# Kernel tuning notes

Measured on AMD Instinct MI355X. Metric: run time of the kernel, lower is better.

Reference implementation:

```python
import jax, jax.numpy as jnp
import numpy as np

NQ = 8
NL = 3
DIM = 2 ** NQ


def _rx(psi, w, theta):
    # theta: scalar or [B]
    B = psi.shape[0]
    t = jnp.atleast_1d(theta).astype(jnp.float32)
    c = jnp.cos(t / 2)[:, None, None].astype(jnp.complex64)
    s = (-1j * jnp.sin(t / 2))[:, None, None].astype(jnp.complex64)
    p = psi.reshape(B, 2 ** w, 2, -1)
    s0, s1 = p[:, :, 0], p[:, :, 1]
    return jnp.stack([c * s0 + s * s1, s * s0 + c * s1], axis=2).reshape(B, DIM)


def _ry(psi, w, theta):
    B = psi.shape[0]
    t = jnp.atleast_1d(theta).astype(jnp.float32)
    c = jnp.cos(t / 2)[:, None, None].astype(jnp.complex64)
    s = jnp.sin(t / 2)[:, None, None].astype(jnp.complex64)
    p = psi.reshape(B, 2 ** w, 2, -1)
    s0, s1 = p[:, :, 0], p[:, :, 1]
    return jnp.stack([c * s0 - s * s1, s * s0 + c * s1], axis=2).reshape(B, DIM)


def _rz(psi, w, theta):
    B = psi.shape[0]
    t = jnp.atleast_1d(theta).astype(jnp.float32)
    e0 = jnp.exp(-0.5j * t.astype(jnp.complex64))[:, None, None]
    e1 = jnp.exp(0.5j * t.astype(jnp.complex64))[:, None, None]
    p = psi.reshape(B, 2 ** w, 2, -1)
    return jnp.stack([e0 * p[:, :, 0], e1 * p[:, :, 1]], axis=2).reshape(B, DIM)


def _cnot(psi, c, t):
    # control c, target t (wire 0 = most significant axis)
    B = psi.shape[0]
    a, b = (c, t) if c < t else (t, c)
    p = psi.reshape(B, 2 ** a, 2, 2 ** (b - a - 1), 2, -1)
    caxis = 2 if c < t else 4
    taxis = 4 if c < t else 2
    idx = [slice(None)] * 6
    idx[caxis] = 1
    sub = p[tuple(idx)]  # control=1 slab, caxis removed
    fl_axis = taxis - (1 if taxis > caxis else 0)
    p = p.at[tuple(idx)].set(jnp.flip(sub, axis=fl_axis))
    return p.reshape(B, DIM)


# PauliZ signs per wire: [NQ, 2^NQ]
_bits = (np.arange(DIM)[None, :] >> (NQ - 1 - np.arange(NQ)[:, None])) & 1
_Z_SIGNS = jnp.asarray((1 - 2 * _bits).astype(np.float32))


def _quantum_layer(enc, qrx, qry, qrz):
    # enc: [B, NQ] encoding angles; qrx/qry/qrz: [NL, NQ] scalar params
    B = enc.shape[0]
    psi = jnp.zeros((B, DIM), jnp.complex64).at[:, 0].set(1.0)
    for i in range(NQ):
        psi = _rx(psi, i, enc[:, i])
    for l in range(NL):
        for i in range(NQ):
            psi = _rx(psi, i, qrx[l, i])
            psi = _ry(psi, i, qry[l, i])
            psi = _rz(psi, i, qrz[l, i])
        for i in range(NQ - 1):
            psi = _cnot(psi, i, i + 1)
        psi = _cnot(psi, NQ - 1, 0)
    probs = psi.real ** 2 + psi.imag ** 2  # [B, 2^NQ]
    return probs @ _Z_SIGNS.T  # [B, NQ] <Z_i>


def _critic(x, w1, b1, w2, b2, qrx, qry, qrz, w3, b3, w4, b4):
    h = jax.nn.relu(x @ w1 + b1)
    enc = h @ w2 + b2
    ex = _quantum_layer(enc, qrx, qry, qrz)
    h2 = jax.nn.relu(ex @ w3 + b3)
    return h2 @ w4 + b4


def setup_inputs() -> dict:
    key = jax.random.key(0)
    ks = jax.random.split(key, 32)
    B, OBS, ACT, H = 65536, 96, 32, 256
    D = OBS + ACT

    def lin(k, fin, fout):
        return jax.random.normal(k, (fin, fout), jnp.float32) * (1.0 / np.sqrt(fin))

    inp = {
        'state': jax.random.normal(ks[0], (B, OBS), jnp.float32),
        'action': jax.random.normal(ks[1], (B, ACT), jnp.float32),
    }
    for ci, tag in enumerate(['a', 'b']):
        o = 2 + ci * 15
        inp['w1' + tag] = lin(ks[o + 0], D, H)
        inp['b1' + tag] = jnp.zeros((H,), jnp.float32)
        inp['w2' + tag] = lin(ks[o + 1], H, NQ)
        inp['b2' + tag] = jnp.zeros((NQ,), jnp.float32)
        inp['qrx' + tag] = jax.random.normal(ks[o + 2], (NL, NQ), jnp.float32)
        inp['qry' + tag] = jax.random.normal(ks[o + 3], (NL, NQ), jnp.float32)
        inp['qrz' + tag] = jax.random.normal(ks[o + 4], (NL, NQ), jnp.float32)
        inp['w3' + tag] = lin(ks[o + 5], NQ, H)
        inp['b3' + tag] = jnp.zeros((H,), jnp.float32)
        inp['w4' + tag] = lin(ks[o + 6], H, 1)
        inp['b4' + tag] = jnp.zeros((1,), jnp.float32)
    return inp


def reference(state, action,
              w1a, b1a, w2a, b2a, qrxa, qrya, qrza, w3a, b3a, w4a, b4a,
              w1b, b1b, w2b, b2b, qrxb, qryb, qrzb, w3b, b3b, w4b, b4b):
    x = jnp.concatenate([state, action], axis=1)
    q1 = _critic(x, w1a, b1a, w2a, b2a, qrxa, qrya, qrza, w3a, b3a, w4a, b4a)
    q2 = _critic(x, w1b, b1b, w2b, b2b, qrxb, qryb, qrzb, w3b, b3b, w4b, b4b)
    return (q1, q2)
```

## Files before the change

kernel.cpp:

```cpp
#include <hip/hip_runtime.h>
#include <math.h>


typedef __attribute__((ext_vector_type(8))) short bfrag_t;
typedef __attribute__((ext_vector_type(16))) float accv_t;

__device__ __forceinline__ unsigned short f2bf(float x) {
  unsigned u = __float_as_uint(x);
  u += 0x7FFFu + ((u >> 16) & 1u);
  return (unsigned short)(u >> 16);
}
__device__ __forceinline__ float bf2f(unsigned short h) {
  return __uint_as_float(((unsigned)h) << 16);
}
__device__ __forceinline__ unsigned pack2(float a, float b) {
  return (unsigned)f2bf(a) | ((unsigned)f2bf(b) << 16);
}

struct C2 { float r, i; };
__device__ __forceinline__ C2 cmul(C2 a, C2 b){ return C2{a.r*b.r - a.i*b.i, a.r*b.i + a.i*b.r}; }
__device__ __forceinline__ C2 cadd(C2 a, C2 b){ return C2{a.r+b.r, a.i+b.i}; }

#define APPLY2(A,Bx)                                                        \
  { float ar=re[A], ai=im[A], br=re[Bx], bi=im[Bx];                         \
    re[A]  = u00r*ar - u00i*ai + u01r*br - u01i*bi;                         \
    im[A]  = u00r*ai + u00i*ar + u01r*bi + u01i*br;                         \
    re[Bx] = u10r*ar - u10i*ai + u11r*br - u11i*bi;                         \
    im[Bx] = u10r*ai + u10i*ar + u11r*bi + u11i*br; }

__global__ __launch_bounds__(256)
void prep_weights(const float* __restrict__ qrxa, const float* __restrict__ qrya,
                  const float* __restrict__ qrza,
                  const float* __restrict__ qrxb, const float* __restrict__ qryb,
                  const float* __restrict__ qrzb,
                  const float* __restrict__ w1a, const float* __restrict__ w1b,
                  const float* __restrict__ w2a, const float* __restrict__ w2b,
                  const float* __restrict__ w3a, const float* __restrict__ w3b,
                  unsigned short* __restrict__ Bm, unsigned short* __restrict__ Gm,
                  unsigned short* __restrict__ w1p, unsigned short* __restrict__ w2p) {
  int blk = blockIdx.x;
  int tid = threadIdx.x;
  if (blk < 128) {
    __shared__ float sg[192];
    int c = blk >> 6;
    if (tid < 24) {
      const float* qx = c ? qrxb : qrxa;
      const float* qy = c ? qryb : qrya;
      const float* qz = c ? qrzb : qrza;
      int g = tid;
      float tx = 0.5f*qx[g], ty = 0.5f*qy[g], tz = 0.5f*qz[g];
      float cx = cosf(tx), sx = sinf(tx);
      float cy = cosf(ty), sy = sinf(ty);
      float cz = cosf(tz), sz = sinf(tz);
      C2 rx00{cx,0.f}, rx01{0.f,-sx}, rx10{0.f,-sx}, rx11{cx,0.f};
      C2 m00 = cadd(cmul(C2{cy,0.f},rx00), cmul(C2{-sy,0.f},rx10));
      C2 m01 = cadd(cmul(C2{cy,0.f},rx01), cmul(C2{-sy,0.f},rx11));
      C2 m10 = cadd(cmul(C2{sy,0.f},rx00), cmul(C2{cy,0.f},rx10));
      C2 m11 = cadd(cmul(C2{sy,0.f},rx01), cmul(C2{cy,0.f},rx11));
      C2 e0{cz,-sz}, e1{cz,sz};
      C2 u00 = cmul(e0,m00), u01 = cmul(e0,m01), u10 = cmul(e1,m10), u11 = cmul(e1,m11);
      float* o = sg + g*8;
      o[0]=u00.r; o[1]=u00.i; o[2]=u01.r; o[3]=u01.i;
      o[4]=u10.r; o[5]=u10.i; o[6]=u11.r; o[7]=u11.i;
    }
    __syncthreads();
    int lane = tid & 63;
    int wid = blk*4 + (tid >> 6);
    int bcol = wid & 255;
    int p = __popc(bcol) & 3;
    float phr = (p==0) ? 1.f : ((p==2) ? -1.f : 0.f);
    float phi = (p==1) ? -1.f : ((p==3) ? 1.f : 0.f);
    float re[4], im[4];
    #pragma unroll
    for (int j = 0; j < 4; ++j) {
      int idx = 4*lane + j;
      re[j] = (idx==bcol) ? phr : 0.f;
      im[j] = (idx==bcol) ? phi : 0.f;
    }
    #pragma unroll
    for (int l = 0; l < 3; ++l) {
      #pragma unroll
      for (int q = 0; q < 8; ++q) {
        const float* u = &sg[(size_t)(l*8 + q)*8];
        float u00r=u[0],u00i=u[1],u01r=u[2],u01i=u[3];
        float u10r=u[4],u10i=u[5],u11r=u[6],u11i=u[7];
        if (q < 6) {
          int m = 5-q, mask = 1<<m;
          bool s1 = ((lane >> m) & 1) != 0;
          float udr = s1?u11r:u00r, udi = s1?u11i:u00i;
          float uor = s1?u10r:u01r, uoi = s1?u10i:u01i;
          #pragma unroll
          for (int j = 0; j < 4; ++j) {
            float pr = __shfl_xor(re[j], mask);
            float pi = __shfl_xor(im[j], mask);
            float nr = udr*re[j] - udi*im[j] + uor*pr - uoi*pi;
            float ni = udr*im[j] + udi*re[j] + uor*pi + uoi*pr;
            re[j]=nr; im[j]=ni;
          }
        } else if (q == 6) { APPLY2(0,2); APPLY2(1,3); }
        else               { APPLY2(0,1); APPLY2(2,3); }
      }
      #pragma unroll
      for (int cq = 0; cq <= 4; ++cq) {
        int tmask = 1 << (4-cq);
        bool pred = ((lane >> (5-cq)) & 1) != 0;
        #pragma unroll
        for (int j = 0; j < 4; ++j) {
          float sr = __shfl_xor(re[j], tmask);
          float si = __shfl_xor(im[j], tmask);
          re[j] = pred ? sr : re[j];
          im[j] = pred ? si : im[j];
        }
      }
      { bool pred = (lane & 1) != 0;
        float t0, t1;
        t0 = pred?re[2]:re[0]; t1 = pred?re[0]:re[2]; re[0]=t0; re[2]=t1;
        t0 = pred?im[2]:im[0]; t1 = pred?im[0]:im[2]; im[0]=t0; im[2]=t1;
        t0 = pred?re[3]:re[1]; t1 = pred?re[1]:re[3]; re[1]=t0; re[3]=t1;
        t0 = pred?im[3]:im[1]; t1 = pred?im[1]:im[3]; im[1]=t0; im[3]=t1; }
      { float t;
        t=re[2]; re[2]=re[3]; re[3]=t;
        t=im[2]; im[2]=im[3]; im[3]=t; }
      { re[1]=__shfl_xor(re[1],32); im[1]=__shfl_xor(im[1],32);
        re[3]=__shfl_xor(re[3],32); im[3]=__shfl_xor(im[3],32); }
    }
    #pragma unroll
    for (int j = 0; j < 4; ++j) {
      int i = 4*lane + j;
      Bm[(size_t)(c*512 + i)*256 + bcol]       = f2bf(re[j]);
      Bm[(size_t)(c*512 + 256 + i)*256 + bcol] = f2bf(im[j]);
    }
  } else if (blk < 192) {
    int slot = (blk-128)*256 + tid;
    int n = slot & 255, h5 = (slot>>8)&1, ks = (slot>>9)&7, p = (slot>>12)&1, c = slot>>13;
    const float* w1c = c ? w1b : w1a;
    #pragma unroll
    for (int j = 0; j < 8; ++j) {
      float v = w1c[(size_t)(ks*16 + h5*8 + j)*256 + n];
      unsigned short hi = f2bf(v);
      w1p[(size_t)slot*8 + j] = p ? f2bf(v - bf2f(hi)) : hi;
    }
  } else if (blk < 200) {
    int slot = (blk-192)*256 + tid;
    int combo = slot >> 4, part = slot & 15;
    int h5 = combo&1, k16 = (combo>>1)&15, p = (combo>>5)&1, c = (combo>>6)&1;
    const float* w2c = c ? w2b : w2a;
    #pragma unroll
    for (int jj = 0; jj < 16; ++jj) {
      int idx = part*16 + jj;
      int il = idx >> 3, j = idx & 7;
      int n = k16*16 + h5*8 + j;
      float v = (il < 8) ? w2c[(size_t)n*8 + il] : 0.f;
      unsigned short hi = f2bf(v);
      w2p[(size_t)combo*256 + idx] = p ? f2bf(v - bf2f(hi)) : hi;
    }
  } else {
    int idx = (blk-200)*256 + tid;
    int c = idx >> 16, w = (idx >> 13) & 7, ks = (idx >> 9) & 15;
    int l = (idx >> 3) & 63, j = idx & 7;
    int n = 32*w + (l & 31);
    int i = ks*16 + (l >> 5)*8 + j;
    const float* w3 = c ? w3b : w3a;
    float s = 0.f;
    #pragma unroll
    for (int q = 0; q < 8; ++q) {
      float sg2 = ((i >> (7-q)) & 1) ? -1.f : 1.f;
      s += sg2 * w3[q*256 + n];
    }
    Gm[idx] = f2bf(s);
  }
}

__global__ __launch_bounds__(256, 2)
void enc_mfma(const float* __restrict__ state, const float* __restrict__ action,
              const unsigned short* __restrict__ w1p,
              const float* __restrict__ b1a, const float* __restrict__ b1b,
              const unsigned short* __restrict__ w2p,
              const float* __restrict__ b2a, const float* __restrict__ b2b,
              float* __restrict__ enc, int Bn) {
  __shared__ __align__(16) char Bx[2][16384];
  __shared__ __align__(16) float sb1[2][256];
  __shared__ float sb2[2][8];
  __shared__ __align__(16) float encw[4][2][32][8];
  int tid = threadIdx.x;
  int lane = tid & 63, w = tid >> 6, il = lane & 31, h5 = lane >> 5;
  int r0 = blockIdx.x * 64;

  sb1[0][tid] = b1a[tid];
  sb1[1][tid] = b1b[tid];
  if (tid < 8) { sb2[0][tid] = b2a[tid]; sb2[1][tid] = b2b[tid]; }

  {
    int m = tid >> 2, kq = tid & 3;
    const float4* st4 = (const float4*)state;
    const float4* ac4 = (const float4*)action;
    #pragma unroll
    for (int ks = 0; ks < 8; ++ks) {
      float4 v = (ks < 6) ? st4[(size_t)(r0+m)*24 + ks*4 + kq]
                          : ac4[(size_t)(r0+m)*8 + (ks-6)*4 + kq];
      unsigned short hx = f2bf(v.x), hy = f2bf(v.y), hz = f2bf(v.z), hw = f2bf(v.w);
      uint2 hh, ll;
      hh.x = (unsigned)hx | ((unsigned)hy << 16);
      hh.y = (unsigned)hz | ((unsigned)hw << 16);
      ll.x = (unsigned)f2bf(v.x - bf2f(hx)) | ((unsigned)f2bf(v.y - bf2f(hy)) << 16);
      ll.y = (unsigned)f2bf(v.z - bf2f(hz)) | ((unsigned)f2bf(v.w - bf2f(hw)) << 16);
      int off = ks*2048 + m*32 + kq*8;
      *(uint2*)(&Bx[0][off]) = hh;
      *(uint2*)(&Bx[1][off]) = ll;
    }
  }
  __syncthreads();

  for (int c = 0; c < 2; ++c) {
    accv_t A[2][2] = {{{},{}},{{},{}}};
    #pragma unroll
    for (int ks = 0; ks < 8; ++ks) {
      bfrag_t a0h, a0l, a1h, a1l;
      {
        size_t b0 = ((size_t)((c*2+0)*8 + ks)*2 + h5)*256;
        size_t b1 = ((size_t)((c*2+1)*8 + ks)*2 + h5)*256;
        int t0 = 2*w, t1 = 2*w+1;
        a0h = *(const bfrag_t*)(w1p + (b0 + t0*32 + il)*8);
        a0l = *(const bfrag_t*)(w1p + (b1 + t0*32 + il)*8);
        a1h = *(const bfrag_t*)(w1p + (b0 + t1*32 + il)*8);
        a1l = *(const bfrag_t*)(w1p + (b1 + t1*32 + il)*8);
      }
      bfrag_t b0h = *(const bfrag_t*)(&Bx[0][ks*2048 + il*32 + h5*16]);
      bfrag_t b0l = *(const bfrag_t*)(&Bx[1][ks*2048 + il*32 + h5*16]);
      bfrag_t b1h_ = *(const bfrag_t*)(&Bx[0][ks*2048 + (32+il)*32 + h5*16]);
      bfrag_t b1l_ = *(const bfrag_t*)(&Bx[1][ks*2048 + (32+il)*32 + h5*16]);
      A[0][0] = __builtin_amdgcn_mfma_f32_32x32x16_bf16(a0h, b0h, A[0][0], 0,0,0);
      A[0][0] = __builtin_amdgcn_mfma_f32_32x32x16_bf16(a0h, b0l, A[0][0], 0,0,0);
      A[0][0] = __builtin_amdgcn_mfma_f32_32x32x16_bf16(a0l, b0h, A[0][0], 0,0,0);
      A[0][1] = __builtin_amdgcn_mfma_f32_32x32x16_bf16(a0h, b1h_, A[0][1], 0,0,0);
      A[0][1] = __builtin_amdgcn_mfma_f32_32x32x16_bf16(a0h, b1l_, A[0][1], 0,0,0);
      A[0][1] = __builtin_amdgcn_mfma_f32_32x32x16_bf16(a0l, b1h_, A[0][1], 0,0,0);
      A[1][0] = __builtin_amdgcn_mfma_f32_32x32x16_bf16(a1h, b0h, A[1][0], 0,0,0);
      A[1][0] = __builtin_amdgcn_mfma_f32_32x32x16_bf16(a1h, b0l, A[1][0], 0,0,0);
      A[1][0] = __builtin_amdgcn_mfma_f32_32x32x16_bf16(a1l, b0h, A[1][0], 0,0,0);
      A[1][1] = __builtin_amdgcn_mfma_f32_32x32x16_bf16(a1h, b1h_, A[1][1], 0,0,0);
      A[1][1] = __builtin_amdgcn_mfma_f32_32x32x16_bf16(a1h, b1l_, A[1][1], 0,0,0);
      A[1][1] = __builtin_amdgcn_mfma_f32_32x32x16_bf16(a1l, b1h_, A[1][1], 0,0,0);
    }
    #pragma unroll
    for (int nt = 0; nt < 2; ++nt) {
      #pragma unroll
      for (int g = 0; g < 4; ++g) {
        float4 bb = *(const float4*)&sb1[c][(2*w+nt)*32 + 8*g + 4*h5];
        float bba[4] = {bb.x, bb.y, bb.z, bb.w};
        #pragma unroll
        for (int jj = 0; jj < 4; ++jj) {
          A[nt][0][4*g+jj] = fmaxf(A[nt][0][4*g+jj] + bba[jj], 0.f);
          A[nt][1][4*g+jj] = fmaxf(A[nt][1][4*g+jj] + bba[jj], 0.f);
        }
      }
    }
    accv_t Cm[2] = {{},{}};
    #pragma unroll
    for (int k2 = 0; k2 < 4; ++k2) {
      int k16 = 4*w + k2;
      bfrag_t g2h = *(const bfrag_t*)(w2p + ((size_t)((c*2+0)*16 + k16)*2 + h5)*256 + il*8);
      bfrag_t g2l = *(const bfrag_t*)(w2p + ((size_t)((c*2+1)*16 + k16)*2 + h5)*256 + il*8);
      #pragma unroll
      for (int mt = 0; mt < 2; ++mt) {
        unsigned ph[2][2], pl[2][2];
        #pragma unroll
        for (int gi = 0; gi < 2; ++gi) {
          int G = 2*k2 + gi, nt = G >> 2, g = G & 3;
          float f0 = A[nt][mt][4*g+0], f1 = A[nt][mt][4*g+1];
          float f2 = A[nt][mt][4*g+2], f3 = A[nt][mt][4*g+3];
          unsigned short h0 = f2bf(f0), h1 = f2bf(f1), h2 = f2bf(f2), h3 = f2bf(f3);
          ph[gi][0] = (unsigned)h0 | ((unsigned)h1 << 16);
          ph[gi][1] = (unsigned)h2 | ((unsigned)h3 << 16);
          pl[gi][0] = (unsigned)f2bf(f0 - bf2f(h0)) | ((unsigned)f2bf(f1 - bf2f(h1)) << 16);
          pl[gi][1] = (unsigned)f2bf(f2 - bf2f(h2)) | ((unsigned)f2bf(f3 - bf2f(h3)) << 16);
        }
        union { bfrag_t v; unsigned u[4]; } FH, FL;
        #pragma unroll
        for (int r = 0; r < 2; ++r) {
          unsigned own_h = h5 ? ph[1][r] : ph[0][r];
          unsigned alt_h = h5 ? ph[0][r] : ph[1][r];
          unsigned rec_h = __shfl_xor((int)alt_h, 32);
          FH.u[r]   = h5 ? rec_h : own_h;
          FH.u[2+r] = h5 ? own_h : rec_h;
          unsigned own_l = h5 ? pl[1][r] : pl[0][r];
          unsigned alt_l = h5 ? pl[0][r] : pl[1][r];
          unsigned rec_l = __shfl_xor((int)alt_l, 32);
          FL.u[r]   = h5 ? rec_l : own_l;
          FL.u[2+r] = h5 ? own_l : rec_l;
        }
        Cm[mt] = __builtin_amdgcn_mfma_f32_32x32x16_bf16(g2h, FH.v, Cm[mt], 0,0,0);
        Cm[mt] = __builtin_amdgcn_mfma_f32_32x32x16_bf16(g2h, FL.v, Cm[mt], 0,0,0);
        Cm[mt] = __builtin_amdgcn_mfma_f32_32x32x16_bf16(g2l, FH.v, Cm[mt], 0,0,0);
      }
    }
    *(float4*)&encw[w][0][il][4*h5] = make_float4(Cm[0][0], Cm[0][1], Cm[0][2], Cm[0][3]);
    *(float4*)&encw[w][1][il][4*h5] = make_float4(Cm[1][0], Cm[1][1], Cm[1][2], Cm[1][3]);
    __syncthreads();
    #pragma unroll
    for (int half = 0; half < 2; ++half) {
      int s = tid + half*256;
      int e = s & 7, mm = s >> 3;
      float v = sb2[c][e];
      #pragma unroll
      for (int ww = 0; ww < 4; ++ww) v += encw[ww][mm>>5][mm&31][e];
      enc[((size_t)c*Bn + r0 + mm)*8 + e] = v;
    }
    __syncthreads();
  }
}

__global__ __launch_bounds__(512, 2)
void qgemm(const float* __restrict__ enc,
           const unsigned short* __restrict__ Bm, const unsigned short* __restrict__ Gm,
           const float* __restrict__ b3a, const float* __restrict__ w4a, const float* __restrict__ b4a,
           const float* __restrict__ b3b, const float* __restrict__ w4b, const float* __restrict__ b4b,
           float* __restrict__ out, int Bn) {
  __shared__ __align__(16) char APq[32768];
  char* Alds = APq;
  char* Plds = APq + 16384;
  float* qtmp = (float*)APq;

  int tid = threadIdx.x;
  int lane = tid & 63;
  int w = tid >> 6;
  int il = lane & 31;
  int h5 = lane >> 5;

  int c = blockIdx.x >> 7;
  int rowblock = blockIdx.x & 127;
  int rowsPerBlock = Bn >> 7;
  int subtiles = rowsPerBlock >> 5;

  bfrag_t bf0[16], bf1[16];
  {
    const unsigned short* base = Bm + ((size_t)(c*512 + 32*w + il)*256 + h5*8);
    #pragma unroll
    for (int ks = 0; ks < 16; ++ks) {
      bf0[ks] = *(const bfrag_t*)(base + ks*16);
      bf1[ks] = *(const bfrag_t*)(base + 256*256 + ks*16);
    }
  }
  int n2 = 32*w + il;
  const float* b3c = c ? b3b : b3a;
  const float* w4c = c ? w4b : w4a;
  const float* b4c = c ? b4b : b4a;
  float b3v = b3c[n2];
  float w4v = w4c[n2];
  float b4v = b4c[0];
  const unsigned short* Gbase = Gm + ((size_t)(c*8 + w)*16)*512 + lane*8;
  int pwbase = (n2>>4)*1024 + ((n2>>3)&1)*512 + (n2&7)*2;
  int rowAdd = 4*h5;

  for (int st = 0; st < subtiles; ++st) {
    int r0 = rowblock*rowsPerBlock + st*32;
    __syncthreads();
    {
      int m = tid & 31, g2 = tid >> 5;
      const float* ep = enc + ((size_t)c*Bn + r0 + m)*8;
      float4 ea = *(const float4*)ep;
      float4 eb = *(const float4*)(ep + 4);
      float c0,s0,c1,s1,c2,s2,c3,s3,c4,s4,c5,s5,c6,s6,c7,s7;
      __sincosf(0.5f*ea.x, &s0, &c0);
      __sincosf(0.5f*ea.y, &s1, &c1);
      __sincosf(0.5f*ea.z, &s2, &c2);
      __sincosf(0.5f*ea.w, &s3, &c3);
      __sincosf(0.5f*eb.x, &s4, &c4);
      __sincosf(0.5f*eb.y, &s5, &c5);
      __sincosf(0.5f*eb.z, &s6, &c6);
      __sincosf(0.5f*eb.w, &s7, &c7);
      float v0 = (g2&8) ? s0 : c0;
      float v1 = (g2&4) ? s1 : c1;
      float v2 = (g2&2) ? s2 : c2;
      float v3 = (g2&1) ? s3 : c3;
      float top = v0*v1*v2*v3;
      float hA = top*c4, hB = top*s4;
      float p67[4];
      p67[0] = c6*c7; p67[1] = c6*s7; p67[2] = s6*c7; p67[3] = s6*s7;
      float low[8];
      #pragma unroll
      for (int j = 0; j < 8; ++j) low[j] = ((j&4) ? s5 : c5) * p67[j&3];
      union { bfrag_t v; unsigned u[4]; } pk;
      #pragma unroll
      for (int k = 0; k < 4; ++k) pk.u[k] = pack2(hA*low[2*k], hA*low[2*k+1]);
      *(bfrag_t*)(Alds + g2*1024 + m*16) = pk.v;
      #pragma unroll
      for (int k = 0; k < 4; ++k) pk.u[k] = pack2(hB*low[2*k], hB*low[2*k+1]);
      *(bfrag_t*)(Alds + g2*1024 + 512 + m*16) = pk.v;
    }
    __syncthreads();
    accv_t acc0 = {}, acc1 = {};
    #pragma unroll
    for (int ks = 0; ks < 16; ++ks) {
      bfrag_t af = *(const bfrag_t*)(Alds + ks*1024 + lane*16);
      acc0 = __builtin_amdgcn_mfma_f32_32x32x16_bf16(af, bf0[ks], acc0, 0, 0, 0);
      acc1 = __builtin_amdgcn_mfma_f32_32x32x16_bf16(af, bf1[ks], acc1, 0, 0, 0);
    }
    #pragma unroll
    for (int r = 0; r < 16; ++r) {
      float P = acc0[r]*acc0[r] + acc1[r]*acc1[r];
      int row = (r&3) + 8*(r>>2) + rowAdd;
      *(unsigned short*)(Plds + pwbase + row*16) = f2bf(P);
    }
    __syncthreads();
    accv_t acc2 = {};
    #pragma unroll 4
    for (int ks = 0; ks < 16; ++ks) {
      bfrag_t pf = *(const bfrag_t*)(Plds + ks*1024 + lane*16);
      bfrag_t gf = *(const bfrag_t*)(Gbase + ks*512);
      acc2 = __builtin_amdgcn_mfma_f32_32x32x16_bf16(pf, gf, acc2, 0, 0, 0);
    }
    float qp[16];
    #pragma unroll
    for (int r = 0; r < 16; ++r) qp[r] = fmaxf(acc2[r] + b3v, 0.f) * w4v;
    __syncthreads();
    #pragma unroll
    for (int r = 0; r < 16; ++r) {
      int row = (r&3) + 8*(r>>2) + rowAdd;
      qtmp[row*256 + n2] = qp[r];
    }
    __syncthreads();
    {
      int row = tid >> 4, seg = tid & 15;
      const float4* qp4 = (const float4*)(qtmp + row*256 + seg*16);
      float4 a0 = qp4[0], a1 = qp4[1], a2 = qp4[2], a3 = qp4[3];
      float s = (a0.x+a0.y+a0.z+a0.w) + (a1.x+a1.y+a1.z+a1.w)
              + (a2.x+a2.y+a2.z+a2.w) + (a3.x+a3.y+a3.z+a3.w);
      s += __shfl_xor(s, 1);
      s += __shfl_xor(s, 2);
      s += __shfl_xor(s, 4);
      s += __shfl_xor(s, 8);
      if (seg == 0) out[(size_t)c*Bn + r0 + row] = s + b4v;
    }
  }
}

extern "C" void kernel_launch(void* const* d_in, const int* in_sizes, int n_in,
                              void* d_out, int out_size, void* d_ws, size_t ws_size,
                              hipStream_t stream) {
  (void)n_in; (void)out_size; (void)ws_size;
  const float* state  = (const float*)d_in[0];
  const float* action = (const float*)d_in[1];
  const float* w1a=(const float*)d_in[2];  const float* b1a=(const float*)d_in[3];
  const float* w2a=(const float*)d_in[4];  const float* b2a=(const float*)d_in[5];
  const float* qrxa=(const float*)d_in[6]; const float* qrya=(const float*)d_in[7];
  const float* qrza=(const float*)d_in[8];
  const float* w3a=(const float*)d_in[9];  const float* b3a=(const float*)d_in[10];
  const float* w4a=(const float*)d_in[11]; const float* b4a=(const float*)d_in[12];
  const float* w1b=(const float*)d_in[13]; const float* b1b=(const float*)d_in[14];
  const float* w2b=(const float*)d_in[15]; const float* b2b=(const float*)d_in[16];
  const float* qrxb=(const float*)d_in[17];const float* qryb=(const float*)d_in[18];
  const float* qrzb=(const float*)d_in[19];
  const float* w3b=(const float*)d_in[20]; const float* b3b=(const float*)d_in[21];
  const float* w4b=(const float*)d_in[22]; const float* b4b=(const float*)d_in[23];

  int B = in_sizes[0] / 96;
  char* wsb = (char*)d_ws;
  unsigned short* Bmat = (unsigned short*)(wsb);
  unsigned short* Gmat = (unsigned short*)(wsb + 524288);
  unsigned short* w1p  = (unsigned short*)(wsb + 786432);
  unsigned short* w2p  = (unsigned short*)(wsb + 1048576);
  float* enc           = (float*)(wsb + 1114112);

  prep_weights<<<712, 256, 0, stream>>>(qrxa,qrya,qrza,qrxb,qryb,qrzb,
                                        w1a,w1b,w2a,w2b,w3a,w3b,
                                        Bmat,Gmat,w1p,w2p);
  enc_mfma<<<B/64, 256, 0, stream>>>(state,action,w1p,b1a,b1b,w2p,b2a,b2b,enc,B);
  qgemm<<<256, 512, 0, stream>>>(enc, Bmat, Gmat, b3a, w4a, b4a, b3b, w4b, b4b,
                                 (float*)d_out, B);
}
```

Measured before the change: 226.4 us.

## Double qgemm grid, pad LDS tiles, prefetch enc rows, de-conflict reduction reads

The qgemm launch grows from 256 to 512 blocks, so each block handles half as many rows and more of the GPU's compute units get work. LDS row strides go from 1024 to 1056 bytes to reduce bank conflicts on the A and P tiles. The enc loads for the next subtile are issued right after the barrier so their latency overlaps the MFMA work. The final row reduction now uses an interleaved float4 pattern to avoid LDS conflicts. In exchange, each block reloads the 32 B-fragments per register, doubling the total B-matrix traffic, and it needs slightly more LDS.

```diff
diff --git a/kernel.cpp b/kernel.cpp
--- a/kernel.cpp
+++ b/kernel.cpp
@@ -316,9 +316,9 @@
            const float* __restrict__ b3a, const float* __restrict__ w4a, const float* __restrict__ b4a,
            const float* __restrict__ b3b, const float* __restrict__ w4b, const float* __restrict__ b4b,
            float* __restrict__ out, int Bn) {
-  __shared__ __align__(16) char APq[32768];
+  __shared__ __align__(16) char APq[33792];
   char* Alds = APq;
-  char* Plds = APq + 16384;
+  char* Plds = APq + 16896;
   float* qtmp = (float*)APq;
 
   int tid = threadIdx.x;
@@ -327,9 +327,9 @@
   int il = lane & 31;
   int h5 = lane >> 5;
 
-  int c = blockIdx.x >> 7;
-  int rowblock = blockIdx.x & 127;
-  int rowsPerBlock = Bn >> 7;
+  int c = blockIdx.x >> 8;
+  int rowblock = blockIdx.x & 255;
+  int rowsPerBlock = Bn >> 8;
   int subtiles = rowsPerBlock >> 5;
 
   bfrag_t bf0[16], bf1[16];
@@ -349,17 +349,22 @@
   float w4v = w4c[n2];
   float b4v = b4c[0];
   const unsigned short* Gbase = Gm + ((size_t)(c*8 + w)*16)*512 + lane*8;
-  int pwbase = (n2>>4)*1024 + ((n2>>3)&1)*512 + (n2&7)*2;
+  int pwbase = (n2>>4)*1056 + ((n2>>3)&1)*512 + (n2&7)*2;
   int rowAdd = 4*h5;
+
+  int am = tid & 31, ag2 = tid >> 5;
+  const float* encb = enc + ((size_t)c*Bn)*8;
+  float4 ea, eb;
+  {
+    const float* ep = encb + (size_t)(rowblock*rowsPerBlock + am)*8;
+    ea = *(const float4*)ep;
+    eb = *(const float4*)(ep + 4);
+  }
 
   for (int st = 0; st < subtiles; ++st) {
     int r0 = rowblock*rowsPerBlock + st*32;
     __syncthreads();
     {
-      int m = tid & 31, g2 = tid >> 5;
-      const float* ep = enc + ((size_t)c*Bn + r0 + m)*8;
-      float4 ea = *(const float4*)ep;
-      float4 eb = *(const float4*)(ep + 4);
       float c0,s0,c1,s1,c2,s2,c3,s3,c4,s4,c5,s5,c6,s6,c7,s7;
       __sincosf(0.5f*ea.x, &s0, &c0);
       __sincosf(0.5f*ea.y, &s1, &c1);
@@ -369,10 +374,10 @@
       __sincosf(0.5f*eb.y, &s5, &c5);
       __sincosf(0.5f*eb.z, &s6, &c6);
       __sincosf(0.5f*eb.w, &s7, &c7);
-      float v0 = (g2&8) ? s0 : c0;
-      float v1 = (g2&4) ? s1 : c1;
-      float v2 = (g2&2) ? s2 : c2;
-      float v3 = (g2&1) ? s3 : c3;
+      float v0 = (ag2&8) ? s0 : c0;
+      float v1 = (ag2&4) ? s1 : c1;
+      float v2 = (ag2&2) ? s2 : c2;
+      float v3 = (ag2&1) ? s3 : c3;
       float top = v0*v1*v2*v3;
       float hA = top*c4, hB = top*s4;
       float p67[4];
@@ -383,16 +388,21 @@
       union { bfrag_t v; unsigned u[4]; } pk;
       #pragma unroll
       for (int k = 0; k < 4; ++k) pk.u[k] = pack2(hA*low[2*k], hA*low[2*k+1]);
-      *(bfrag_t*)(Alds + g2*1024 + m*16) = pk.v;
+      *(bfrag_t*)(Alds + ag2*1056 + am*16) = pk.v;
       #pragma unroll
       for (int k = 0; k < 4; ++k) pk.u[k] = pack2(hB*low[2*k], hB*low[2*k+1]);
-      *(bfrag_t*)(Alds + g2*1024 + 512 + m*16) = pk.v;
-    }
-    __syncthreads();
+      *(bfrag_t*)(Alds + ag2*1056 + 512 + am*16) = pk.v;
+    }
+    __syncthreads();
+    if (st + 1 < subtiles) {
+      const float* ep = encb + (size_t)(r0 + 32 + am)*8;
+      ea = *(const float4*)ep;
+      eb = *(const float4*)(ep + 4);
+    }
     accv_t acc0 = {}, acc1 = {};
     #pragma unroll
     for (int ks = 0; ks < 16; ++ks) {
-      bfrag_t af = *(const bfrag_t*)(Alds + ks*1024 + lane*16);
+      bfrag_t af = *(const bfrag_t*)(Alds + ks*1056 + lane*16);
       acc0 = __builtin_amdgcn_mfma_f32_32x32x16_bf16(af, bf0[ks], acc0, 0, 0, 0);
       acc1 = __builtin_amdgcn_mfma_f32_32x32x16_bf16(af, bf1[ks], acc1, 0, 0, 0);
     }
@@ -406,7 +416,7 @@
     accv_t acc2 = {};
     #pragma unroll 4
     for (int ks = 0; ks < 16; ++ks) {
-      bfrag_t pf = *(const bfrag_t*)(Plds + ks*1024 + lane*16);
+      bfrag_t pf = *(const bfrag_t*)(Plds + ks*1056 + lane*16);
       bfrag_t gf = *(const bfrag_t*)(Gbase + ks*512);
       acc2 = __builtin_amdgcn_mfma_f32_32x32x16_bf16(pf, gf, acc2, 0, 0, 0);
     }
@@ -422,10 +432,13 @@
     __syncthreads();
     {
       int row = tid >> 4, seg = tid & 15;
-      const float4* qp4 = (const float4*)(qtmp + row*256 + seg*16);
-      float4 a0 = qp4[0], a1 = qp4[1], a2 = qp4[2], a3 = qp4[3];
-      float s = (a0.x+a0.y+a0.z+a0.w) + (a1.x+a1.y+a1.z+a1.w)
-              + (a2.x+a2.y+a2.z+a2.w) + (a3.x+a3.y+a3.z+a3.w);
+      const float* qrow = qtmp + row*256;
+      float s = 0.f;
+      #pragma unroll
+      for (int j = 0; j < 4; ++j) {
+        float4 a = *(const float4*)(qrow + j*64 + seg*4);
+        s += (a.x + a.y) + (a.z + a.w);
+      }
       s += __shfl_xor(s, 1);
       s += __shfl_xor(s, 2);
       s += __shfl_xor(s, 4);
@@ -466,6 +479,6 @@
                                         w1a,w1b,w2a,w2b,w3a,w3b,
                                         Bmat,Gmat,w1p,w2p);
   enc_mfma<<<B/64, 256, 0, stream>>>(state,action,w1p,b1a,b1b,w2p,b2a,b2b,enc,B);
-  qgemm<<<256, 512, 0, stream>>>(enc, Bmat, Gmat, b3a, w4a, b4a, b3b, w4b, b4b,
+  qgemm<<<512, 512, 0, stream>>>(enc, Bmat, Gmat, b3a, w4a, b4a, b3b, w4b, b4b,
                                  (float*)d_out, B);
 }
```

Result: no change. 229.2 us (+1.2%).

## Build state-vector GEMM operands in registers and process two row subtiles per iteration

Applied to the files above, without the earlier changes.

The first-stage A fragments (encoded product states) are now built directly in each lane's registers and fed to MFMA, removing the A LDS write/read and one barrier. Each loop iteration now handles two 32-row subtiles with separate padded P buffers, sharing the G fragment loads across two MFMAs. The final row reduction uses 8 lanes per row with a rotated read order to avoid bank conflicts. LDS use grows to about 99KB per block, which may stop two 512-thread blocks from sharing a CU, and each wave recomputes the sincos terms redundantly.

```diff
diff --git a/kernel.cpp b/kernel.cpp
--- a/kernel.cpp
+++ b/kernel.cpp
@@ -310,16 +310,59 @@
   }
 }
 
+__device__ __forceinline__ void stage1_reg(const float* __restrict__ ep, int h5,
+                                           const bfrag_t* bf0, const bfrag_t* bf1,
+                                           char* P, int pwbase, int rowAdd) {
+  float4 ea = *(const float4*)ep;
+  float4 eb = *(const float4*)(ep + 4);
+  float c0,s0,c1,s1,c2,s2,c3,s3,c4,s4,c5,s5,c6,s6,c7,s7;
+  __sincosf(0.5f*ea.x, &s0, &c0);
+  __sincosf(0.5f*ea.y, &s1, &c1);
+  __sincosf(0.5f*ea.z, &s2, &c2);
+  __sincosf(0.5f*ea.w, &s3, &c3);
+  __sincosf(0.5f*eb.x, &s4, &c4);
+  __sincosf(0.5f*eb.y, &s5, &c5);
+  __sincosf(0.5f*eb.z, &s6, &c6);
+  __sincosf(0.5f*eb.w, &s7, &c7);
+  float p67[4];
+  p67[0] = c6*c7; p67[1] = c6*s7; p67[2] = s6*c7; p67[3] = s6*s7;
+  float low[8];
+  #pragma unroll
+  for (int j = 0; j < 8; ++j) low[j] = ((j&4) ? s5 : c5) * p67[j&3];
+  float h45 = h5 ? s4 : c4;
+  accv_t acc0 = {}, acc1 = {};
+  #pragma unroll
+  for (int ks = 0; ks < 16; ++ks) {
+    float v0 = (ks&8) ? s0 : c0;
+    float v1 = (ks&4) ? s1 : c1;
+    float v2 = (ks&2) ? s2 : c2;
+    float v3 = (ks&1) ? s3 : c3;
+    float top = v0*v1*v2*v3;
+    float hA = top*h45;
+    union { bfrag_t v; unsigned u[4]; } af;
+    #pragma unroll
+    for (int k = 0; k < 4; ++k) af.u[k] = pack2(hA*low[2*k], hA*low[2*k+1]);
+    acc0 = __builtin_amdgcn_mfma_f32_32x32x16_bf16(af.v, bf0[ks], acc0, 0, 0, 0);
+    acc1 = __builtin_amdgcn_mfma_f32_32x32x16_bf16(af.v, bf1[ks], acc1, 0, 0, 0);
+  }
+  #pragma unroll
+  for (int r = 0; r < 16; ++r) {
+    float Pv = acc0[r]*acc0[r] + acc1[r]*acc1[r];
+    int row = (r&3) + 8*(r>>2) + rowAdd;
+    *(unsigned short*)(P + pwbase + row*16) = f2bf(Pv);
+  }
+}
+
 __global__ __launch_bounds__(512, 2)
 void qgemm(const float* __restrict__ enc,
            const unsigned short* __restrict__ Bm, const unsigned short* __restrict__ Gm,
            const float* __restrict__ b3a, const float* __restrict__ w4a, const float* __restrict__ b4a,
            const float* __restrict__ b3b, const float* __restrict__ w4b, const float* __restrict__ b4b,
            float* __restrict__ out, int Bn) {
-  __shared__ __align__(16) char APq[32768];
-  char* Alds = APq;
-  char* Plds = APq + 16384;
-  float* qtmp = (float*)APq;
+  __shared__ __align__(16) char APq[98816];
+  char* P0 = APq;
+  char* P1 = APq + 16640;
+  float* qtmp = (float*)(APq + 33280);
 
   int tid = threadIdx.x;
   int lane = tid & 63;
@@ -330,7 +373,7 @@
   int c = blockIdx.x >> 7;
   int rowblock = blockIdx.x & 127;
   int rowsPerBlock = Bn >> 7;
-  int subtiles = rowsPerBlock >> 5;
+  int npairs = rowsPerBlock >> 6;
 
   bfrag_t bf0[16], bf1[16];
   {
@@ -349,87 +392,47 @@
   float w4v = w4c[n2];
   float b4v = b4c[0];
   const unsigned short* Gbase = Gm + ((size_t)(c*8 + w)*16)*512 + lane*8;
-  int pwbase = (n2>>4)*1024 + ((n2>>3)&1)*512 + (n2&7)*2;
+  int pwbase = (n2>>4)*1040 + ((n2>>3)&1)*528 + (n2&7)*2;
+  int prd = il*16 + h5*528;
   int rowAdd = 4*h5;
 
-  for (int st = 0; st < subtiles; ++st) {
-    int r0 = rowblock*rowsPerBlock + st*32;
+  const float* encb = enc + ((size_t)c*Bn)*8;
+  int rbase = rowblock*rowsPerBlock;
+
+  for (int st2 = 0; st2 < npairs; ++st2) {
+    int r0 = rbase + st2*64;
+    stage1_reg(encb + (size_t)(r0 + il)*8,      h5, bf0, bf1, P0, pwbase, rowAdd);
+    stage1_reg(encb + (size_t)(r0 + 32 + il)*8, h5, bf0, bf1, P1, pwbase, rowAdd);
+    __syncthreads();
+    accv_t acc2a = {}, acc2b = {};
+    #pragma unroll 4
+    for (int ks = 0; ks < 16; ++ks) {
+      bfrag_t gf  = *(const bfrag_t*)(Gbase + ks*512);
+      bfrag_t pf0 = *(const bfrag_t*)(P0 + ks*1040 + prd);
+      bfrag_t pf1 = *(const bfrag_t*)(P1 + ks*1040 + prd);
+      acc2a = __builtin_amdgcn_mfma_f32_32x32x16_bf16(pf0, gf, acc2a, 0, 0, 0);
+      acc2b = __builtin_amdgcn_mfma_f32_32x32x16_bf16(pf1, gf, acc2b, 0, 0, 0);
+    }
+    #pragma unroll
+    for (int r = 0; r < 16; ++r) {
+      int row = (r&3) + 8*(r>>2) + rowAdd;
+      qtmp[row*256 + n2]        = fmaxf(acc2a[r] + b3v, 0.f) * w4v;
+      qtmp[(32 + row)*256 + n2] = fmaxf(acc2b[r] + b3v, 0.f) * w4v;
+    }
     __syncthreads();
     {
-      int m = tid & 31, g2 = tid >> 5;
-      const float* ep = enc + ((size_t)c*Bn + r0 + m)*8;
-      float4 ea = *(const float4*)ep;
-      float4 eb = *(const float4*)(ep + 4);
-      float c0,s0,c1,s1,c2,s2,c3,s3,c4,s4,c5,s5,c6,s6,c7,s7;
-      __sincosf(0.5f*ea.x, &s0, &c0);
-      __sincosf(0.5f*ea.y, &s1, &c1);
-      __sincosf(0.5f*ea.z, &s2, &c2);
-      __sincosf(0.5f*ea.w, &s3, &c3);
-      __sincosf(0.5f*eb.x, &s4, &c4);
-      __sincosf(0.5f*eb.y, &s5, &c5);
-      __sincosf(0.5f*eb.z, &s6, &c6);
-      __sincosf(0.5f*eb.w, &s7, &c7);
-      float v0 = (g2&8) ? s0 : c0;
-      float v1 = (g2&4) ? s1 : c1;
-      float v2 = (g2&2) ? s2 : c2;
-      float v3 = (g2&1) ? s3 : c3;
-      float top = v0*v1*v2*v3;
-      float hA = top*c4, hB = top*s4;
-      float p67[4];
-      p67[0] = c6*c7; p67[1] = c6*s7; p67[2] = s6*c7; p67[3] = s6*s7;
-      float low[8];
-      #pragma unroll
-      for (int j = 0; j < 8; ++j) low[j] = ((j&4) ? s5 : c5) * p67[j&3];
-      union { bfrag_t v; unsigned u[4]; } pk;
-      #pragma unroll
-      for (int k = 0; k < 4; ++k) pk.u[k] = pack2(hA*low[2*k], hA*low[2*k+1]);
-      *(bfrag_t*)(Alds + g2*1024 + m*16) = pk.v;
-      #pragma unroll
-      for (int k = 0; k < 4; ++k) pk.u[k] = pack2(hB*low[2*k], hB*low[2*k+1]);
-      *(bfrag_t*)(Alds + g2*1024 + 512 + m*16) = pk.v;
-    }
-    __syncthreads();
-    accv_t acc0 = {}, acc1 = {};
-    #pragma unroll
-    for (int ks = 0; ks < 16; ++ks) {
-      bfrag_t af = *(const bfrag_t*)(Alds + ks*1024 + lane*16);
-      acc0 = __builtin_amdgcn_mfma_f32_32x32x16_bf16(af, bf0[ks], acc0, 0, 0, 0);
-      acc1 = __builtin_amdgcn_mfma_f32_32x32x16_bf16(af, bf1[ks], acc1, 0, 0, 0);
-    }
-    #pragma unroll
-    for (int r = 0; r < 16; ++r) {
-      float P = acc0[r]*acc0[r] + acc1[r]*acc1[r];
-      int row = (r&3) + 8*(r>>2) + rowAdd;
-      *(unsigned short*)(Plds + pwbase + row*16) = f2bf(P);
-    }
-    __syncthreads();
-    accv_t acc2 = {};
-    #pragma unroll 4
-    for (int ks = 0; ks < 16; ++ks) {
-      bfrag_t pf = *(const bfrag_t*)(Plds + ks*1024 + lane*16);
-      bfrag_t gf = *(const bfrag_t*)(Gbase + ks*512);
-      acc2 = __builtin_amdgcn_mfma_f32_32x32x16_bf16(pf, gf, acc2, 0, 0, 0);
-    }
-    float qp[16];
-    #pragma unroll
-    for (int r = 0; r < 16; ++r) qp[r] = fmaxf(acc2[r] + b3v, 0.f) * w4v;
-    __syncthreads();
-    #pragma unroll
-    for (int r = 0; r < 16; ++r) {
-      int row = (r&3) + 8*(r>>2) + rowAdd;
-      qtmp[row*256 + n2] = qp[r];
-    }
-    __syncthreads();
-    {
-      int row = tid >> 4, seg = tid & 15;
-      const float4* qp4 = (const float4*)(qtmp + row*256 + seg*16);
-      float4 a0 = qp4[0], a1 = qp4[1], a2 = qp4[2], a3 = qp4[3];
-      float s = (a0.x+a0.y+a0.z+a0.w) + (a1.x+a1.y+a1.z+a1.w)
-              + (a2.x+a2.y+a2.z+a2.w) + (a3.x+a3.y+a3.z+a3.w);
+      int row = tid >> 3, seg = tid & 7;
+      int sg = (seg + row) & 7;
+      const float* qrow = qtmp + row*256;
+      float s = 0.f;
+      #pragma unroll
+      for (int t = 0; t < 8; ++t) {
+        float4 a = *(const float4*)(qrow + t*32 + sg*4);
+        s += (a.x + a.y) + (a.z + a.w);
+      }
       s += __shfl_xor(s, 1);
       s += __shfl_xor(s, 2);
       s += __shfl_xor(s, 4);
-      s += __shfl_xor(s, 8);
       if (seg == 0) out[(size_t)c*Bn + r0 + row] = s + b4v;
     }
   }
```

After: 228.4 us. No clear change (+0.9%).
